# Kernel tuning notes

Measured on AMD Instinct MI355X. Metric: run time of the kernel, lower is better.

## Reference

```python
import jax, jax.numpy as jnp
import numpy as np

N, E, D = 100000, 1600000, 128
EPS = 1e-5


def _bn(h, g, b):
    m = h.mean(0)
    v = ((h - m) ** 2).mean(0)  # biased var, as torch BatchNorm1d normalization
    return g * (h - m) / jnp.sqrt(v + EPS) + b


def _sage(x, src, dst, w_self, w_neigh, b, n):
    # mean aggregation over in-neighbors (edges src->dst)
    agg = jax.ops.segment_sum(x[src], dst, num_segments=n)          # [N, D]
    cnt = jax.ops.segment_sum(jnp.ones(src.shape, x.dtype), dst, num_segments=n)
    mean = agg / jnp.maximum(cnt, 1.0)[:, None]
    return x @ w_self + mean @ w_neigh + b


def setup_inputs() -> dict:
    key = jax.random.key(0)
    ks = jax.random.split(key, 8)
    s = 1.0 / np.sqrt(D)
    return {
        "x": jax.random.normal(ks[0], (N, D), jnp.float32),
        "src": jax.random.randint(ks[1], (E,), 0, N, jnp.int32),
        "dst": jax.random.randint(ks[2], (E,), 0, N, jnp.int32),
        "w_self1": jax.random.normal(ks[3], (D, D), jnp.float32) * s,
        "w_neigh1": jax.random.normal(ks[4], (D, D), jnp.float32) * s,
        "b1": jnp.zeros((D,), jnp.float32),
        "w_self2": jax.random.normal(ks[5], (D, D), jnp.float32) * s,
        "w_neigh2": jax.random.normal(ks[6], (D, D), jnp.float32) * s,
        "b2": jnp.zeros((D,), jnp.float32),
        "w_skip": jax.random.normal(ks[7], (D, D), jnp.float32) * s,
        "b_skip": jnp.zeros((D,), jnp.float32),
        "g1": jnp.ones((D,), jnp.float32), "be1": jnp.zeros((D,), jnp.float32),
        "g2": jnp.ones((D,), jnp.float32), "be2": jnp.zeros((D,), jnp.float32),
        "g3": jnp.ones((D,), jnp.float32), "be3": jnp.zeros((D,), jnp.float32),
    }


def reference(x, src, dst, w_self1, w_neigh1, b1, w_self2, w_neigh2, b2,
              w_skip, b_skip, g1, be1, g2, be2, g3, be3):
    n = x.shape[0]
    h1 = _sage(x, src, dst, w_self1, w_neigh1, b1, n)
    h1 = jax.nn.relu(_bn(h1, g1, be1))           # dropout: eval-mode identity
    h2 = _sage(h1, src, dst, w_self2, w_neigh2, b2, n)
    h2 = _bn(h2, g2, be2)
    skip = _bn(h1 @ w_skip + b_skip, g3, be3)
    return jax.nn.relu(h2 + skip)
```

## Files before the change

kernel.cpp:

```cpp
#include <hip/hip_runtime.h>

#define D 128
#define PCHUNK 4096
#define SCAP 8192

typedef short bf16x8 __attribute__((ext_vector_type(8)));
typedef float f32x4 __attribute__((ext_vector_type(4)));

__device__ __forceinline__ ushort f2b(float f){
  unsigned u = __builtin_bit_cast(unsigned, f);
  u += 0x7fffu + ((u >> 16) & 1u);
  return (ushort)(u >> 16);
}
__device__ __forceinline__ float b2f(ushort h){
  unsigned u = ((unsigned)h) << 16;
  return __builtin_bit_cast(float, u);
}

__global__ __launch_bounds__(256) void k_p0(const int* __restrict__ dst,
                                            int* __restrict__ bcnt, int E){
  __shared__ int h[512];
  for (int u=threadIdx.x; u<512; u+=256) h[u]=0;
  __syncthreads();
  for (long long i=(long long)blockIdx.x*256+threadIdx.x; i<E; i+=(long long)gridDim.x*256)
    atomicAdd(&h[dst[i]>>8], 1);
  __syncthreads();
  for (int u=threadIdx.x; u<512; u+=256) if (h[u]) atomicAdd(&bcnt[u], h[u]);
}

__global__ void k_bscan(const int* __restrict__ bcnt, int* __restrict__ bbase,
                        int* __restrict__ bcur, int nb, int E){
  __shared__ int sh[1024];
  int t = threadIdx.x;
  int v = (t<nb) ? bcnt[t] : 0;
  sh[t]=v; __syncthreads();
  for (int off=1; off<1024; off<<=1){
    int add = (t>=off)?sh[t-off]:0;
    __syncthreads();
    sh[t]+=add;
    __syncthreads();
  }
  if (t<nb){ int e=sh[t]-v; bbase[t]=e; bcur[t]=e; }
  if (t==nb) bbase[t]=E;
}

__global__ __launch_bounds__(256) void k_part(const int* __restrict__ src,
        const int* __restrict__ dst, int* __restrict__ bcur,
        unsigned* __restrict__ pairs, int E){
  __shared__ int hist[512], offA[512], offB[512], gbase[512];
  __shared__ int sS[PCHUNK], sD[PCHUNK];
  const int t = threadIdx.x;
  const int base = blockIdx.x * PCHUNK;
  const int cnt = min(PCHUNK, E - base);
  for (int u=t; u<512; u+=256) hist[u]=0;
  __syncthreads();
  int rs[16], rd[16];
  #pragma unroll
  for (int j=0;j<16;j++){
    int li = j*256 + t;
    if (li < cnt){
      rs[j]=src[base+li]; rd[j]=dst[base+li];
      atomicAdd(&hist[rd[j]>>8],1);
    } else { rs[j]=0; rd[j]=-1; }
  }
  __syncthreads();
  int *cur=offA, *nxt=offB;
  for (int u=t; u<512; u+=256) cur[u]=hist[u];
  __syncthreads();
  for (int off=1; off<512; off<<=1){
    for (int u=t; u<512; u+=256) nxt[u] = cur[u] + ((u>=off)?cur[u-off]:0);
    __syncthreads();
    int* tmp=cur; cur=nxt; nxt=tmp;
  }
  for (int u=t; u<512; u+=256) nxt[u] = cur[u]-hist[u];
  __syncthreads();
  #pragma unroll
  for (int j=0;j<16;j++){
    if (j*256+t < cnt){
      int b = rd[j]>>8;
      int p = atomicAdd(&nxt[b],1);
      sS[p]=rs[j]; sD[p]=rd[j];
    }
  }
  __syncthreads();
  for (int u=t; u<512; u+=256){
    int c = hist[u];
    if (c>0) gbase[u] = atomicAdd(&bcur[u], c);
  }
  __syncthreads();
  #pragma unroll
  for (int j=0;j<16;j++){
    int idx = j*256+t;
    if (idx<cnt){
      int d = sD[idx]; int b = d>>8;
      int gpos = gbase[b] + (idx - (cur[b]-hist[b]));
      pairs[gpos] = (unsigned)sS[idx] | ((unsigned)(d & 255) << 24);
    }
  }
}

__global__ __launch_bounds__(256) void k_sortb(const unsigned* __restrict__ pairs,
        const int* __restrict__ bbase, int* __restrict__ offs,
        int* __restrict__ slots, int N, int NB){
  __shared__ int nh[256], nc[256], sc[256];
  __shared__ int stage[SCAP];
  const int b = blockIdx.x, t = threadIdx.x;
  const int base = bbase[b];
  const int cnt  = bbase[b+1] - base;
  nh[t]=0; __syncthreads();
  for (int i=t;i<cnt;i+=256) atomicAdd(&nh[pairs[base+i] >> 24],1);
  __syncthreads();
  int v = nh[t];
  sc[t]=v; __syncthreads();
  for (int off=1; off<256; off<<=1){
    int add = (t>=off)?sc[t-off]:0;
    __syncthreads();
    sc[t]+=add;
    __syncthreads();
  }
  int excl = sc[t]-v;
  nc[t]=excl;
  int node = (b<<8)+t;
  if (node<N) offs[node]=base+excl;
  if (b==NB-1 && t==0) offs[N]=bbase[NB];
  __syncthreads();
  if (cnt<=SCAP){
    for (int i=t;i<cnt;i+=256){
      unsigned p = pairs[base+i];
      int pos = atomicAdd(&nc[p >> 24],1);
      stage[pos]=(int)(p & 0xffffffu);
    }
    __syncthreads();
    for (int i=t;i<cnt;i+=256) slots[base+i]=stage[i];
  } else {
    for (int i=t;i<cnt;i+=256){
      unsigned p = pairs[base+i];
      int pos = atomicAdd(&nc[p >> 24],1);
      slots[base+pos]=(int)(p & 0xffffffu);
    }
  }
}

__global__ __launch_bounds__(256) void k_xcast(const float* __restrict__ x,
                                               ushort* __restrict__ xb, long long n4){
  long long i = (long long)blockIdx.x*256 + threadIdx.x;
  const long long stride = (long long)gridDim.x*256;
  for (; i < n4; i += stride){
    float4 v = reinterpret_cast<const float4*>(x)[i];
    ushort4 o;
    o.x = f2b(v.x); o.y = f2b(v.y); o.z = f2b(v.z); o.w = f2b(v.w);
    reinterpret_cast<ushort4*>(xb)[i] = o;
  }
}

__global__ __launch_bounds__(256) void k_wtall(
    const float* __restrict__ w_self1, const float* __restrict__ w_neigh1,
    const float* __restrict__ w_self2, const float* __restrict__ w_neigh2,
    const float* __restrict__ w_skip,
    ushort* __restrict__ Wb1, ushort* __restrict__ Wb2, ushort* __restrict__ Wb3){
  const int grp = blockIdx.x >> 6;
  const int idx = (blockIdx.x & 63)*256 + threadIdx.x;
  const int k = idx >> 7, c = idx & 127;
  const float* W; ushort* Wb; int K, k0;
  switch (grp){
    case 0: W=w_self1;  Wb=Wb1; K=256; k0=0;   break;
    case 1: W=w_neigh1; Wb=Wb1; K=256; k0=128; break;
    case 2: W=w_self2;  Wb=Wb2; K=256; k0=0;   break;
    case 3: W=w_neigh2; Wb=Wb2; K=256; k0=128; break;
    default:W=w_skip;   Wb=Wb3; K=128; k0=0;   break;
  }
  Wb[(size_t)c*K + k0 + k] = f2b(W[idx]);
}

__global__ __launch_bounds__(256) void k_gatherb(const ushort* __restrict__ Xb,
        const int* __restrict__ slots, const int* __restrict__ offs,
        ushort* __restrict__ meanb, int N){
  int node = blockIdx.x*4 + (threadIdx.x >> 6);
  int c2 = (threadIdx.x & 63) * 2;
  if (node >= N) return;
  const int beg = offs[node], end = offs[node+1];
  float sx0=0,sy0=0,sx1=0,sy1=0,sx2=0,sy2=0,sx3=0,sy3=0;
  int j = beg;
  while (j < end && (j & 3)){
    unsigned u = *reinterpret_cast<const unsigned*>(&Xb[(size_t)slots[j]*D + c2]);
    sx0 += b2f((ushort)u); sy0 += b2f((ushort)(u>>16));
    ++j;
  }
  const int nfull = (end - j) >> 2;
  const int4* sp = reinterpret_cast<const int4*>(slots + j);

#define G8(ia, ib) { \
    unsigned u0 = *reinterpret_cast<const unsigned*>(&Xb[(size_t)(ia).x*D + c2]); \
    unsigned u1 = *reinterpret_cast<const unsigned*>(&Xb[(size_t)(ia).y*D + c2]); \
    unsigned u2 = *reinterpret_cast<const unsigned*>(&Xb[(size_t)(ia).z*D + c2]); \
    unsigned u3 = *reinterpret_cast<const unsigned*>(&Xb[(size_t)(ia).w*D + c2]); \
    unsigned u4 = *reinterpret_cast<const unsigned*>(&Xb[(size_t)(ib).x*D + c2]); \
    unsigned u5 = *reinterpret_cast<const unsigned*>(&Xb[(size_t)(ib).y*D + c2]); \
    unsigned u6 = *reinterpret_cast<const unsigned*>(&Xb[(size_t)(ib).z*D + c2]); \
    unsigned u7 = *reinterpret_cast<const unsigned*>(&Xb[(size_t)(ib).w*D + c2]); \
    sx0 += b2f((ushort)u0); sy0 += b2f((ushort)(u0>>16)); \
    sx1 += b2f((ushort)u1); sy1 += b2f((ushort)(u1>>16)); \
    sx2 += b2f((ushort)u2); sy2 += b2f((ushort)(u2>>16)); \
    sx3 += b2f((ushort)u3); sy3 += b2f((ushort)(u3>>16)); \
    sx0 += b2f((ushort)u4); sy0 += b2f((ushort)(u4>>16)); \
    sx1 += b2f((ushort)u5); sy1 += b2f((ushort)(u5>>16)); \
    sx2 += b2f((ushort)u6); sy2 += b2f((ushort)(u6>>16)); \
    sx3 += b2f((ushort)u7); sy3 += b2f((ushort)(u7>>16)); }

  int g = 0;
  if (nfull >= 2){
    int4 ia = sp[0], ib = sp[1];
    for (g = 2; g + 2 <= nfull; g += 2){
      int4 na = sp[g], nb = sp[g+1];
      G8(ia, ib);
      ia = na; ib = nb;
    }
    G8(ia, ib);
  }
  if (g < nfull){
    int4 ia = sp[g];
    unsigned u0 = *reinterpret_cast<const unsigned*>(&Xb[(size_t)ia.x*D + c2]);
    unsigned u1 = *reinterpret_cast<const unsigned*>(&Xb[(size_t)ia.y*D + c2]);
    unsigned u2 = *reinterpret_cast<const unsigned*>(&Xb[(size_t)ia.z*D + c2]);
    unsigned u3 = *reinterpret_cast<const unsigned*>(&Xb[(size_t)ia.w*D + c2]);
    sx0 += b2f((ushort)u0); sy0 += b2f((ushort)(u0>>16));
    sx1 += b2f((ushort)u1); sy1 += b2f((ushort)(u1>>16));
    sx2 += b2f((ushort)u2); sy2 += b2f((ushort)(u2>>16));
    sx3 += b2f((ushort)u3); sy3 += b2f((ushort)(u3>>16));
  }
  j += 4*nfull;
  for (; j < end; ++j){
    unsigned u = *reinterpret_cast<const unsigned*>(&Xb[(size_t)slots[j]*D + c2]);
    sx0 += b2f((ushort)u); sy0 += b2f((ushort)(u>>16));
  }
#undef G8
  float deg = (float)(end - beg);
  float rc = deg > 0.f ? 1.0f/deg : 0.f;
  unsigned o = (unsigned)f2b((sx0+sx1+sx2+sx3)*rc)
             | ((unsigned)f2b((sy0+sy1+sy2+sy3)*rc) << 16);
  *reinterpret_cast<unsigned*>(&meanb[(size_t)node*D + c2]) = o;
}

template<bool SKIP>
__global__ __launch_bounds__(256, 2) void k_mfma(
    const ushort* __restrict__ A0, const ushort* __restrict__ A1,
    const ushort* __restrict__ Wb, const ushort* __restrict__ Wk,
    const float* __restrict__ bias, const float* __restrict__ biasK,
    ushort* __restrict__ C, ushort* __restrict__ Ck,
    float* __restrict__ gS, float* __restrict__ gQ,
    float* __restrict__ gSK, float* __restrict__ gQK, int N, int NT)
{
  __shared__ ushort At[2][64][40];
  __shared__ ushort Wt[2][128][40];
  __shared__ ushort Wkt[SKIP ? 2*128*40 : 1];
  __shared__ float shS[128], shQ[128], shSK[SKIP?128:1], shQK[SKIP?128:1];
  const int tid = threadIdx.x;
  if (tid < 128){ shS[tid]=0.f; shQ[tid]=0.f; if (SKIP){ shSK[tid]=0.f; shQK[tid]=0.f; } }
  const int bid = blockIdx.x, gridN = gridDim.x;
  const int lane = tid & 63, wid = tid >> 6;
  const int wr = wid >> 1, wc = wid & 1;
  const int lr = lane & 15, kq = lane >> 4;
  const int srA = tid >> 2, s8A = (tid & 3) * 8;
  const int srW = tid >> 2, s8W = (tid & 3) * 8;

  int4 va0, va1, va2, va3;
  int4 w0a,w0b, w1a,w1b, w2a,w2b, w3a,w3b;
  int4 k0a,k0b, k1a,k1b, k2a,k2b, k3a,k3b;

#define LOADSET(S, GT, TT) { \
    int grow_ = (GT)*64 + srA; if (grow_ >= N) grow_ = N-1; \
    const ushort* As_ = ((TT) >= 4) ? A1 : A0; \
    va##S = *reinterpret_cast<const int4*>(&As_[(size_t)grow_*D + ((TT)&3)*32 + s8A]); \
    w##S##a = *reinterpret_cast<const int4*>(&Wb[(size_t)srW*256 + (TT)*32 + s8W]); \
    w##S##b = *reinterpret_cast<const int4*>(&Wb[(size_t)(srW+64)*256 + (TT)*32 + s8W]); \
    if (SKIP && (TT) < 4){ \
      k##S##a = *reinterpret_cast<const int4*>(&Wk[(size_t)srW*128 + (TT)*32 + s8W]); \
      k##S##b = *reinterpret_cast<const int4*>(&Wk[(size_t)(srW+64)*128 + (TT)*32 + s8W]); \
    } }

#define WRITESET(S, BW, TT) { \
    *reinterpret_cast<int4*>(&At[BW][srA][s8A]) = va##S; \
    *reinterpret_cast<int4*>(&Wt[BW][srW][s8W]) = w##S##a; \
    *reinterpret_cast<int4*>(&Wt[BW][srW+64][s8W]) = w##S##b; \
    if (SKIP && (TT) < 4){ \
      *reinterpret_cast<int4*>(&Wkt[((BW)*128 + srW)*40 + s8W]) = k##S##a; \
      *reinterpret_cast<int4*>(&Wkt[((BW)*128 + srW + 64)*40 + s8W]) = k##S##b; \
    } }

#define PBAR() { asm volatile("s_waitcnt lgkmcnt(0)" ::: "memory"); \
    __builtin_amdgcn_s_barrier(); __builtin_amdgcn_sched_barrier(0); }

#define STEPBODY(BR, WITHK, ...) { \
    bf16x8 af0 = *reinterpret_cast<const bf16x8*>(&At[BR][32*wr + lr][kq*8]); \
    bf16x8 af1 = *reinterpret_cast<const bf16x8*>(&At[BR][32*wr + 16 + lr][kq*8]); \
    bf16x8 bw0 = *reinterpret_cast<const bf16x8*>(&Wt[BR][64*wc + lr][kq*8]); \
    bf16x8 bw1 = *reinterpret_cast<const bf16x8*>(&Wt[BR][64*wc + 16 + lr][kq*8]); \
    bf16x8 bw2 = *reinterpret_cast<const bf16x8*>(&Wt[BR][64*wc + 32 + lr][kq*8]); \
    bf16x8 bw3 = *reinterpret_cast<const bf16x8*>(&Wt[BR][64*wc + 48 + lr][kq*8]); \
    bf16x8 bk0{}, bk1{}, bk2{}, bk3{}; \
    if (SKIP && (WITHK)){ \
      bk0 = *reinterpret_cast<const bf16x8*>(&Wkt[((BR)*128 + 64*wc + lr)*40 + kq*8]); \
      bk1 = *reinterpret_cast<const bf16x8*>(&Wkt[((BR)*128 + 64*wc + 16 + lr)*40 + kq*8]); \
      bk2 = *reinterpret_cast<const bf16x8*>(&Wkt[((BR)*128 + 64*wc + 32 + lr)*40 + kq*8]); \
      bk3 = *reinterpret_cast<const bf16x8*>(&Wkt[((BR)*128 + 64*wc + 48 + lr)*40 + kq*8]); \
    } \
    __VA_ARGS__; \
    __builtin_amdgcn_s_setprio(1); \
    acc[0][0] = __builtin_amdgcn_mfma_f32_16x16x32_bf16(af0, bw0, acc[0][0], 0,0,0); \
    acc[0][1] = __builtin_amdgcn_mfma_f32_16x16x32_bf16(af0, bw1, acc[0][1], 0,0,0); \
    acc[0][2] = __builtin_amdgcn_mfma_f32_16x16x32_bf16(af0, bw2, acc[0][2], 0,0,0); \
    acc[0][3] = __builtin_amdgcn_mfma_f32_16x16x32_bf16(af0, bw3, acc[0][3], 0,0,0); \
    acc[1][0] = __builtin_amdgcn_mfma_f32_16x16x32_bf16(af1, bw0, acc[1][0], 0,0,0); \
    acc[1][1] = __builtin_amdgcn_mfma_f32_16x16x32_bf16(af1, bw1, acc[1][1], 0,0,0); \
    acc[1][2] = __builtin_amdgcn_mfma_f32_16x16x32_bf16(af1, bw2, acc[1][2], 0,0,0); \
    acc[1][3] = __builtin_amdgcn_mfma_f32_16x16x32_bf16(af1, bw3, acc[1][3], 0,0,0); \
    if (SKIP && (WITHK)){ \
      accK[0][0] = __builtin_amdgcn_mfma_f32_16x16x32_bf16(af0, bk0, accK[0][0], 0,0,0); \
      accK[0][1] = __builtin_amdgcn_mfma_f32_16x16x32_bf16(af0, bk1, accK[0][1], 0,0,0); \
      accK[0][2] = __builtin_amdgcn_mfma_f32_16x16x32_bf16(af0, bk2, accK[0][2], 0,0,0); \
      accK[0][3] = __builtin_amdgcn_mfma_f32_16x16x32_bf16(af0, bk3, accK[0][3], 0,0,0); \
      accK[1][0] = __builtin_amdgcn_mfma_f32_16x16x32_bf16(af1, bk0, accK[1][0], 0,0,0); \
      accK[1][1] = __builtin_amdgcn_mfma_f32_16x16x32_bf16(af1, bk1, accK[1][1], 0,0,0); \
      accK[1][2] = __builtin_amdgcn_mfma_f32_16x16x32_bf16(af1, bk2, accK[1][2], 0,0,0); \
      accK[1][3] = __builtin_amdgcn_mfma_f32_16x16x32_bf16(af1, bk3, accK[1][3], 0,0,0); \
    } \
    __builtin_amdgcn_s_setprio(0); }

  f32x4 acc[2][4], accK[SKIP?2:1][SKIP?4:1];
  #pragma unroll
  for (int m=0;m<2;m++)
    #pragma unroll
    for (int n=0;n<4;n++){
      acc[m][n] = (f32x4){0.f,0.f,0.f,0.f};
      if (SKIP) accK[m][n] = (f32x4){0.f,0.f,0.f,0.f};
    }
  float bs[4]={0,0,0,0}, bq[4]={0,0,0,0}, bsk[4]={0,0,0,0}, bqk[4]={0,0,0,0};
  float bv[4], bkv[4];
  #pragma unroll
  for (int n=0;n<4;n++){
    bv[n] = bias[64*wc + 16*n + lr];
    bkv[n] = SKIP ? biasK[64*wc + 16*n + lr] : 0.f;
  }

  {
    const int t0 = bid;
    LOADSET(0, t0, 0);
    LOADSET(1, t0, 1);
    LOADSET(2, t0, 2);
    LOADSET(3, t0, 3);
    WRITESET(0, 0, 0);
    PBAR();
  }

  for (int tile = bid; tile < NT; tile += gridN){
    const int tnext = tile + gridN;
    const bool hasnext = (tnext < NT);
    STEPBODY(0, 1, LOADSET(0, tile, 4));
    WRITESET(1, 1, 1); PBAR();
    STEPBODY(1, 1, LOADSET(1, tile, 5));
    WRITESET(2, 0, 2); PBAR();
    STEPBODY(0, 1, LOADSET(2, tile, 6));
    WRITESET(3, 1, 3); PBAR();
    STEPBODY(1, 1, LOADSET(3, tile, 7));
    WRITESET(0, 0, 4); PBAR();
    STEPBODY(0, 0, if (hasnext) LOADSET(0, tnext, 0));
    WRITESET(1, 1, 5); PBAR();
    STEPBODY(1, 0, if (hasnext) LOADSET(1, tnext, 1));
    WRITESET(2, 0, 6); PBAR();
    STEPBODY(0, 0, if (hasnext) LOADSET(2, tnext, 2));
    WRITESET(3, 1, 7); PBAR();
    STEPBODY(1, 0, if (hasnext) LOADSET(3, tnext, 3));
    if (hasnext){ WRITESET(0, 0, 0); PBAR(); }

    #pragma unroll
    for (int m=0;m<2;m++){
      #pragma unroll
      for (int r=0;r<4;r++){
        int row = tile*64 + 32*wr + 16*m + kq*4 + r;
        if (row < N){
          #pragma unroll
          for (int n=0;n<4;n++){
            int col = 64*wc + 16*n + lr;
            float v = acc[m][n][r] + bv[n];
            C[(size_t)row*D + col] = f2b(v);
            bs[n] += v; bq[n] += v*v;
            if (SKIP){
              float u = accK[m][n][r] + bkv[n];
              Ck[(size_t)row*D + col] = f2b(u);
              bsk[n] += u; bqk[n] += u*u;
            }
          }
        }
      }
    }
    #pragma unroll
    for (int m=0;m<2;m++)
      #pragma unroll
      for (int n=0;n<4;n++){
        acc[m][n] = (f32x4){0.f,0.f,0.f,0.f};
        if (SKIP) accK[m][n] = (f32x4){0.f,0.f,0.f,0.f};
      }
  }
#undef LOADSET
#undef WRITESET
#undef PBAR
#undef STEPBODY

  #pragma unroll
  for (int n=0;n<4;n++){
    float s = bs[n], q = bq[n];
    s += __shfl_xor(s,16); s += __shfl_xor(s,32);
    q += __shfl_xor(q,16); q += __shfl_xor(q,32);
    if (kq == 0){
      int col = 64*wc + 16*n + lr;
      atomicAdd(&shS[col], s);
      atomicAdd(&shQ[col], q);
    }
    if (SKIP){
      float sk = bsk[n], qk = bqk[n];
      sk += __shfl_xor(sk,16); sk += __shfl_xor(sk,32);
      qk += __shfl_xor(qk,16); qk += __shfl_xor(qk,32);
      if (kq == 0){
        int col = 64*wc + 16*n + lr;
        atomicAdd(&shSK[col], sk);
        atomicAdd(&shQK[col], qk);
      }
    }
  }
  __syncthreads();
  if (tid < 128){
    unsafeAtomicAdd(&gS[tid], shS[tid]);
    unsafeAtomicAdd(&gQ[tid], shQ[tid]);
    if (SKIP){
      unsafeAtomicAdd(&gSK[tid], shSK[tid]);
      unsafeAtomicAdd(&gQK[tid], shQK[tid]);
    }
  }
}

__global__ __launch_bounds__(256) void k_bnrelub(const ushort* __restrict__ hpre,
      ushort* __restrict__ hb,
      const float* __restrict__ sum, const float* __restrict__ sq,
      const float* __restrict__ g, const float* __restrict__ be,
      float invN, long long n4){
  __shared__ float A[128], B[128];
  if (threadIdx.x < 128){
    int c = threadIdx.x;
    float m = sum[c]*invN;
    float v = sq[c]*invN - m*m;
    float a = g[c]*rsqrtf(fmaxf(v, 0.f) + 1e-5f);
    A[c] = a;
    B[c] = be[c] - m*a;
  }
  __syncthreads();
  long long i = (long long)blockIdx.x*256 + threadIdx.x;
  const long long stride = (long long)gridDim.x*256;
  for (; i < n4; i += stride){
    int c = ((int)(i & 31)) << 2;
    float4 a = *reinterpret_cast<const float4*>(A + c);
    float4 b = *reinterpret_cast<const float4*>(B + c);
    ushort4 hv = reinterpret_cast<const ushort4*>(hpre)[i];
    ushort4 o;
    o.x = f2b(fmaxf(a.x*b2f(hv.x) + b.x, 0.f));
    o.y = f2b(fmaxf(a.y*b2f(hv.y) + b.y, 0.f));
    o.z = f2b(fmaxf(a.z*b2f(hv.z) + b.z, 0.f));
    o.w = f2b(fmaxf(a.w*b2f(hv.w) + b.w, 0.f));
    reinterpret_cast<ushort4*>(hb)[i] = o;
  }
}

__global__ __launch_bounds__(256) void k_final(const ushort* __restrict__ h2,
      const ushort* __restrict__ sk, float* __restrict__ out,
      const float* __restrict__ sum2, const float* __restrict__ sq2,
      const float* __restrict__ g2, const float* __restrict__ be2,
      const float* __restrict__ sum3, const float* __restrict__ sq3,
      const float* __restrict__ g3, const float* __restrict__ be3,
      float invN, long long n4){
  __shared__ float A2[128], B2[128], A3[128], B3[128];
  if (threadIdx.x < 128){
    int c = threadIdx.x;
    float m2 = sum2[c]*invN;
    float v2 = sq2[c]*invN - m2*m2;
    float a2 = g2[c]*rsqrtf(fmaxf(v2, 0.f) + 1e-5f);
    A2[c] = a2; B2[c] = be2[c] - m2*a2;
    float m3 = sum3[c]*invN;
    float v3 = sq3[c]*invN - m3*m3;
    float a3 = g3[c]*rsqrtf(fmaxf(v3, 0.f) + 1e-5f);
    A3[c] = a3; B3[c] = be3[c] - m3*a3;
  }
  __syncthreads();
  long long i = (long long)blockIdx.x*256 + threadIdx.x;
  const long long stride = (long long)gridDim.x*256;
  for (; i < n4; i += stride){
    int c = ((int)(i & 31)) << 2;
    float4 a2 = *reinterpret_cast<const float4*>(A2 + c);
    float4 b2 = *reinterpret_cast<const float4*>(B2 + c);
    float4 a3 = *reinterpret_cast<const float4*>(A3 + c);
    float4 b3 = *reinterpret_cast<const float4*>(B3 + c);
    ushort4 h = reinterpret_cast<const ushort4*>(h2)[i];
    ushort4 s = reinterpret_cast<const ushort4*>(sk)[i];
    float4 v;
    v.x = fmaxf(a2.x*b2f(h.x) + b2.x + a3.x*b2f(s.x) + b3.x, 0.f);
    v.y = fmaxf(a2.y*b2f(h.y) + b2.y + a3.y*b2f(s.y) + b3.y, 0.f);
    v.z = fmaxf(a2.z*b2f(h.z) + b2.z + a3.z*b2f(s.z) + b3.z, 0.f);
    v.w = fmaxf(a2.w*b2f(h.w) + b2.w + a3.w*b2f(s.w) + b3.w, 0.f);
    reinterpret_cast<float4*>(out)[i] = v;
  }
}

extern "C" void kernel_launch(void* const* d_in, const int* in_sizes, int n_in,
                              void* d_out, int out_size, void* d_ws, size_t ws_size,
                              hipStream_t stream) {
  const float* x        = (const float*)d_in[0];
  const int*   src      = (const int*)  d_in[1];
  const int*   dst      = (const int*)  d_in[2];
  const float* w_self1  = (const float*)d_in[3];
  const float* w_neigh1 = (const float*)d_in[4];
  const float* b1       = (const float*)d_in[5];
  const float* w_self2  = (const float*)d_in[6];
  const float* w_neigh2 = (const float*)d_in[7];
  const float* b2       = (const float*)d_in[8];
  const float* w_skip   = (const float*)d_in[9];
  const float* b_skip   = (const float*)d_in[10];
  const float* g1       = (const float*)d_in[11];
  const float* be1      = (const float*)d_in[12];
  const float* g2       = (const float*)d_in[13];
  const float* be2      = (const float*)d_in[14];
  const float* g3       = (const float*)d_in[15];
  const float* be3      = (const float*)d_in[16];
  (void)n_in; (void)ws_size;

  const int N = in_sizes[0] / D;
  const int E = in_sizes[1];
  const int NB = (N + 255) >> 8;
  float* out = (float*)d_out;

  char* p = (char*)d_ws;
  const size_t nd2 = (((size_t)N * D * 2) + 255) / 256 * 256;
  ushort* meanb  = (ushort*)p; p += nd2;
  ushort* h1b    = (ushort*)p; p += nd2;
  ushort* hpre_b = (ushort*)p; p += nd2;
  ushort* skip_b = (ushort*)p; p += nd2;
  ushort* Wb1    = (ushort*)p; p += 256*128*2;
  ushort* Wb2    = (ushort*)p; p += 256*128*2;
  ushort* Wb3    = (ushort*)p; p += 128*128*2;
  int*    offs   = (int*)p;   p += (((size_t)(N+1)*4) + 255) / 256 * 256;
  int*    bcnt   = (int*)p;   p += 2304;
  float*  st     = (float*)p; p += 1536*sizeof(float);
  int*    bbase  = (int*)p;   p += 2304;
  int*    bcur   = (int*)p;   p += 2048;
  float *sum1=st,      *sq1=st+128,  *sum2=st+256, *sq2=st+384, *sum3=st+512, *sq3=st+640;

  const size_t slpad = (((size_t)E*4) + 255) / 256 * 256;
  const size_t xbpad = (((size_t)N*D*2) + 255) / 256 * 256;
  int*      slots = (int*)d_out;
  ushort*   xb    = (ushort*)((char*)d_out + slpad);
  unsigned* pairs = (unsigned*)((char*)d_out + slpad + xbpad);

  hipMemsetAsync(bcnt, 0, 2304 + 1536*sizeof(float), stream);

  const long long n4 = (long long)N * D / 4;

  k_xcast<<<2048, 256, 0, stream>>>(x, xb, n4);
  k_wtall<<<320, 256, 0, stream>>>(w_self1, w_neigh1, w_self2, w_neigh2, w_skip,
                                   Wb1, Wb2, Wb3);

  k_p0<<<1024, 256, 0, stream>>>(dst, bcnt, E);
  k_bscan<<<1, 1024, 0, stream>>>(bcnt, bbase, bcur, NB, E);
  k_part<<<(E + PCHUNK - 1)/PCHUNK, 256, 0, stream>>>(src, dst, bcur, pairs, E);
  k_sortb<<<NB, 256, 0, stream>>>(pairs, bbase, offs, slots, N, NB);

  const int gablocks = (N + 3) / 4;
  const int NT = (N + 63) / 64;
  const int gpersist = 512;
  const float invN = 1.0f / (float)N;

  k_gatherb<<<gablocks, 256, 0, stream>>>(xb, slots, offs, meanb, N);
  k_mfma<false><<<gpersist, 256, 0, stream>>>(xb, meanb, Wb1, nullptr, b1, nullptr,
                                              hpre_b, nullptr, sum1, sq1, nullptr, nullptr, N, NT);
  k_bnrelub<<<4096, 256, 0, stream>>>(hpre_b, h1b, sum1, sq1, g1, be1, invN, n4);

  k_gatherb<<<gablocks, 256, 0, stream>>>(h1b, slots, offs, meanb, N);

  k_mfma<true><<<gpersist, 256, 0, stream>>>(h1b, meanb, Wb2, Wb3, b2, b_skip,
                                             hpre_b, skip_b, sum2, sq2, sum3, sq3, N, NT);

  k_final<<<4096, 256, 0, stream>>>(hpre_b, skip_b, out,
                                    sum2, sq2, g2, be2, sum3, sq3, g3, be3, invN, n4);
}
```

Measured before the change: 301.3 us.

## Keep weights resident in LDS and double MFMA row tile to 128

The persistent GEMM kernel now loads the full concatenated weight matrix (and the skip weight) into LDS once per block, instead of streaming weight slices alongside every A tile. The row tile grows from 64 to 128 rows, so each wave computes a 64x64 output block with twice the accumulators. The grid is halved to 256 blocks and launch bounds drop to one block per CU. This cuts redundant global weight loads and LDS writes per tile, at the cost of a large LDS footprint (about 100 KB with skip) and higher register pressure, which lowers occupancy.

```diff
diff --git a/kernel.cpp b/kernel.cpp
--- a/kernel.cpp
+++ b/kernel.cpp
@@ -242,7 +242,7 @@
 }
 
 template<bool SKIP>
-__global__ __launch_bounds__(256, 2) void k_mfma(
+__global__ __launch_bounds__(256, 1) void k_mfma(
     const ushort* __restrict__ A0, const ushort* __restrict__ A1,
     const ushort* __restrict__ Wb, const ushort* __restrict__ Wk,
     const float* __restrict__ bias, const float* __restrict__ biasK,
@@ -250,9 +250,9 @@
     float* __restrict__ gS, float* __restrict__ gQ,
     float* __restrict__ gSK, float* __restrict__ gQK, int N, int NT)
 {
-  __shared__ ushort At[2][64][40];
-  __shared__ ushort Wt[2][128][40];
-  __shared__ ushort Wkt[SKIP ? 2*128*40 : 1];
+  __shared__ ushort Wt8[8][128][40];
+  __shared__ ushort Wkt4[SKIP ? 4*128*40 : 1];
+  __shared__ ushort At[2][128][40];
   __shared__ float shS[128], shQ[128], shSK[SKIP?128:1], shQK[SKIP?128:1];
   const int tid = threadIdx.x;
   if (tid < 128){ shS[tid]=0.f; shQ[tid]=0.f; if (SKIP){ shSK[tid]=0.f; shQK[tid]=0.f; } }
@@ -260,49 +260,57 @@
   const int lane = tid & 63, wid = tid >> 6;
   const int wr = wid >> 1, wc = wid & 1;
   const int lr = lane & 15, kq = lane >> 4;
-  const int srA = tid >> 2, s8A = (tid & 3) * 8;
-  const int srW = tid >> 2, s8W = (tid & 3) * 8;
-
-  int4 va0, va1, va2, va3;
-  int4 w0a,w0b, w1a,w1b, w2a,w2b, w3a,w3b;
-  int4 k0a,k0b, k1a,k1b, k2a,k2b, k3a,k3b;
-
-#define LOADSET(S, GT, TT) { \
-    int grow_ = (GT)*64 + srA; if (grow_ >= N) grow_ = N-1; \
+  const int sr4 = tid >> 2, s8 = (tid & 3) * 8;
+
+  #pragma unroll
+  for (int s=0;s<8;s++){
+    *reinterpret_cast<int4*>(&Wt8[s][sr4][s8]) =
+        *reinterpret_cast<const int4*>(&Wb[(size_t)sr4*256 + s*32 + s8]);
+    *reinterpret_cast<int4*>(&Wt8[s][sr4+64][s8]) =
+        *reinterpret_cast<const int4*>(&Wb[(size_t)(sr4+64)*256 + s*32 + s8]);
+  }
+  if (SKIP){
+    #pragma unroll
+    for (int s=0;s<4;s++){
+      *reinterpret_cast<int4*>(&Wkt4[((s*128) + sr4)*40 + s8]) =
+          *reinterpret_cast<const int4*>(&Wk[(size_t)sr4*128 + s*32 + s8]);
+      *reinterpret_cast<int4*>(&Wkt4[((s*128) + sr4 + 64)*40 + s8]) =
+          *reinterpret_cast<const int4*>(&Wk[(size_t)(sr4+64)*128 + s*32 + s8]);
+    }
+  }
+
+  int4 va0a,va0b, va1a,va1b, va2a,va2b, va3a,va3b;
+
+#define LOADA(S, GT, TT) { \
+    int gr0_ = (GT)*128 + sr4;      if (gr0_ >= N) gr0_ = N-1; \
+    int gr1_ = (GT)*128 + sr4 + 64; if (gr1_ >= N) gr1_ = N-1; \
     const ushort* As_ = ((TT) >= 4) ? A1 : A0; \
-    va##S = *reinterpret_cast<const int4*>(&As_[(size_t)grow_*D + ((TT)&3)*32 + s8A]); \
-    w##S##a = *reinterpret_cast<const int4*>(&Wb[(size_t)srW*256 + (TT)*32 + s8W]); \
-    w##S##b = *reinterpret_cast<const int4*>(&Wb[(size_t)(srW+64)*256 + (TT)*32 + s8W]); \
-    if (SKIP && (TT) < 4){ \
-      k##S##a = *reinterpret_cast<const int4*>(&Wk[(size_t)srW*128 + (TT)*32 + s8W]); \
-      k##S##b = *reinterpret_cast<const int4*>(&Wk[(size_t)(srW+64)*128 + (TT)*32 + s8W]); \
-    } }
-
-#define WRITESET(S, BW, TT) { \
-    *reinterpret_cast<int4*>(&At[BW][srA][s8A]) = va##S; \
-    *reinterpret_cast<int4*>(&Wt[BW][srW][s8W]) = w##S##a; \
-    *reinterpret_cast<int4*>(&Wt[BW][srW+64][s8W]) = w##S##b; \
-    if (SKIP && (TT) < 4){ \
-      *reinterpret_cast<int4*>(&Wkt[((BW)*128 + srW)*40 + s8W]) = k##S##a; \
-      *reinterpret_cast<int4*>(&Wkt[((BW)*128 + srW + 64)*40 + s8W]) = k##S##b; \
-    } }
+    const int ka_ = ((TT) & 3) * 32; \
+    va##S##a = *reinterpret_cast<const int4*>(&As_[(size_t)gr0_*D + ka_ + s8]); \
+    va##S##b = *reinterpret_cast<const int4*>(&As_[(size_t)gr1_*D + ka_ + s8]); }
+
+#define WRITEA(S, BW) { \
+    *reinterpret_cast<int4*>(&At[BW][sr4][s8]) = va##S##a; \
+    *reinterpret_cast<int4*>(&At[BW][sr4+64][s8]) = va##S##b; }
 
 #define PBAR() { asm volatile("s_waitcnt lgkmcnt(0)" ::: "memory"); \
     __builtin_amdgcn_s_barrier(); __builtin_amdgcn_sched_barrier(0); }
 
-#define STEPBODY(BR, WITHK, ...) { \
-    bf16x8 af0 = *reinterpret_cast<const bf16x8*>(&At[BR][32*wr + lr][kq*8]); \
-    bf16x8 af1 = *reinterpret_cast<const bf16x8*>(&At[BR][32*wr + 16 + lr][kq*8]); \
-    bf16x8 bw0 = *reinterpret_cast<const bf16x8*>(&Wt[BR][64*wc + lr][kq*8]); \
-    bf16x8 bw1 = *reinterpret_cast<const bf16x8*>(&Wt[BR][64*wc + 16 + lr][kq*8]); \
-    bf16x8 bw2 = *reinterpret_cast<const bf16x8*>(&Wt[BR][64*wc + 32 + lr][kq*8]); \
-    bf16x8 bw3 = *reinterpret_cast<const bf16x8*>(&Wt[BR][64*wc + 48 + lr][kq*8]); \
+#define STEPBODY(BR, TT, WITHK, ...) { \
+    bf16x8 af0 = *reinterpret_cast<const bf16x8*>(&At[BR][64*wr + lr][kq*8]); \
+    bf16x8 af1 = *reinterpret_cast<const bf16x8*>(&At[BR][64*wr + 16 + lr][kq*8]); \
+    bf16x8 af2 = *reinterpret_cast<const bf16x8*>(&At[BR][64*wr + 32 + lr][kq*8]); \
+    bf16x8 af3 = *reinterpret_cast<const bf16x8*>(&At[BR][64*wr + 48 + lr][kq*8]); \
+    bf16x8 bw0 = *reinterpret_cast<const bf16x8*>(&Wt8[TT][64*wc + lr][kq*8]); \
+    bf16x8 bw1 = *reinterpret_cast<const bf16x8*>(&Wt8[TT][64*wc + 16 + lr][kq*8]); \
+    bf16x8 bw2 = *reinterpret_cast<const bf16x8*>(&Wt8[TT][64*wc + 32 + lr][kq*8]); \
+    bf16x8 bw3 = *reinterpret_cast<const bf16x8*>(&Wt8[TT][64*wc + 48 + lr][kq*8]); \
     bf16x8 bk0{}, bk1{}, bk2{}, bk3{}; \
     if (SKIP && (WITHK)){ \
-      bk0 = *reinterpret_cast<const bf16x8*>(&Wkt[((BR)*128 + 64*wc + lr)*40 + kq*8]); \
-      bk1 = *reinterpret_cast<const bf16x8*>(&Wkt[((BR)*128 + 64*wc + 16 + lr)*40 + kq*8]); \
-      bk2 = *reinterpret_cast<const bf16x8*>(&Wkt[((BR)*128 + 64*wc + 32 + lr)*40 + kq*8]); \
-      bk3 = *reinterpret_cast<const bf16x8*>(&Wkt[((BR)*128 + 64*wc + 48 + lr)*40 + kq*8]); \
+      bk0 = *reinterpret_cast<const bf16x8*>(&Wkt4[(((TT)&3)*128 + 64*wc + lr)*40 + kq*8]); \
+      bk1 = *reinterpret_cast<const bf16x8*>(&Wkt4[(((TT)&3)*128 + 64*wc + 16 + lr)*40 + kq*8]); \
+      bk2 = *reinterpret_cast<const bf16x8*>(&Wkt4[(((TT)&3)*128 + 64*wc + 32 + lr)*40 + kq*8]); \
+      bk3 = *reinterpret_cast<const bf16x8*>(&Wkt4[(((TT)&3)*128 + 64*wc + 48 + lr)*40 + kq*8]); \
     } \
     __VA_ARGS__; \
     __builtin_amdgcn_s_setprio(1); \
@@ -314,6 +322,14 @@
     acc[1][1] = __builtin_amdgcn_mfma_f32_16x16x32_bf16(af1, bw1, acc[1][1], 0,0,0); \
     acc[1][2] = __builtin_amdgcn_mfma_f32_16x16x32_bf16(af1, bw2, acc[1][2], 0,0,0); \
     acc[1][3] = __builtin_amdgcn_mfma_f32_16x16x32_bf16(af1, bw3, acc[1][3], 0,0,0); \
+    acc[2][0] = __builtin_amdgcn_mfma_f32_16x16x32_bf16(af2, bw0, acc[2][0], 0,0,0); \
+    acc[2][1] = __builtin_amdgcn_mfma_f32_16x16x32_bf16(af2, bw1, acc[2][1], 0,0,0); \
+    acc[2][2] = __builtin_amdgcn_mfma_f32_16x16x32_bf16(af2, bw2, acc[2][2], 0,0,0); \
+    acc[2][3] = __builtin_amdgcn_mfma_f32_16x16x32_bf16(af2, bw3, acc[2][3], 0,0,0); \
+    acc[3][0] = __builtin_amdgcn_mfma_f32_16x16x32_bf16(af3, bw0, acc[3][0], 0,0,0); \
+    acc[3][1] = __builtin_amdgcn_mfma_f32_16x16x32_bf16(af3, bw1, acc[3][1], 0,0,0); \
+    acc[3][2] = __builtin_amdgcn_mfma_f32_16x16x32_bf16(af3, bw2, acc[3][2], 0,0,0); \
+    acc[3][3] = __builtin_amdgcn_mfma_f32_16x16x32_bf16(af3, bw3, acc[3][3], 0,0,0); \
     if (SKIP && (WITHK)){ \
       accK[0][0] = __builtin_amdgcn_mfma_f32_16x16x32_bf16(af0, bk0, accK[0][0], 0,0,0); \
       accK[0][1] = __builtin_amdgcn_mfma_f32_16x16x32_bf16(af0, bk1, accK[0][1], 0,0,0); \
@@ -323,12 +339,20 @@
       accK[1][1] = __builtin_amdgcn_mfma_f32_16x16x32_bf16(af1, bk1, accK[1][1], 0,0,0); \
       accK[1][2] = __builtin_amdgcn_mfma_f32_16x16x32_bf16(af1, bk2, accK[1][2], 0,0,0); \
       accK[1][3] = __builtin_amdgcn_mfma_f32_16x16x32_bf16(af1, bk3, accK[1][3], 0,0,0); \
+      accK[2][0] = __builtin_amdgcn_mfma_f32_16x16x32_bf16(af2, bk0, accK[2][0], 0,0,0); \
+      accK[2][1] = __builtin_amdgcn_mfma_f32_16x16x32_bf16(af2, bk1, accK[2][1], 0,0,0); \
+      accK[2][2] = __builtin_amdgcn_mfma_f32_16x16x32_bf16(af2, bk2, accK[2][2], 0,0,0); \
+      accK[2][3] = __builtin_amdgcn_mfma_f32_16x16x32_bf16(af2, bk3, accK[2][3], 0,0,0); \
+      accK[3][0] = __builtin_amdgcn_mfma_f32_16x16x32_bf16(af3, bk0, accK[3][0], 0,0,0); \
+      accK[3][1] = __builtin_amdgcn_mfma_f32_16x16x32_bf16(af3, bk1, accK[3][1], 0,0,0); \
+      accK[3][2] = __builtin_amdgcn_mfma_f32_16x16x32_bf16(af3, bk2, accK[3][2], 0,0,0); \
+      accK[3][3] = __builtin_amdgcn_mfma_f32_16x16x32_bf16(af3, bk3, accK[3][3], 0,0,0); \
     } \
     __builtin_amdgcn_s_setprio(0); }
 
-  f32x4 acc[2][4], accK[SKIP?2:1][SKIP?4:1];
+  f32x4 acc[4][4], accK[SKIP?4:1][SKIP?4:1];
   #pragma unroll
-  for (int m=0;m<2;m++)
+  for (int m=0;m<4;m++)
     #pragma unroll
     for (int n=0;n<4;n++){
       acc[m][n] = (f32x4){0.f,0.f,0.f,0.f};
@@ -344,39 +368,39 @@
 
   {
     const int t0 = bid;
-    LOADSET(0, t0, 0);
-    LOADSET(1, t0, 1);
-    LOADSET(2, t0, 2);
-    LOADSET(3, t0, 3);
-    WRITESET(0, 0, 0);
+    LOADA(0, t0, 0);
+    LOADA(1, t0, 1);
+    LOADA(2, t0, 2);
+    LOADA(3, t0, 3);
+    WRITEA(0, 0);
     PBAR();
   }
 
   for (int tile = bid; tile < NT; tile += gridN){
     const int tnext = tile + gridN;
     const bool hasnext = (tnext < NT);
-    STEPBODY(0, 1, LOADSET(0, tile, 4));
-    WRITESET(1, 1, 1); PBAR();
-    STEPBODY(1, 1, LOADSET(1, tile, 5));
-    WRITESET(2, 0, 2); PBAR();
-    STEPBODY(0, 1, LOADSET(2, tile, 6));
-    WRITESET(3, 1, 3); PBAR();
-    STEPBODY(1, 1, LOADSET(3, tile, 7));
-    WRITESET(0, 0, 4); PBAR();
-    STEPBODY(0, 0, if (hasnext) LOADSET(0, tnext, 0));
-    WRITESET(1, 1, 5); PBAR();
-    STEPBODY(1, 0, if (hasnext) LOADSET(1, tnext, 1));
-    WRITESET(2, 0, 6); PBAR();
-    STEPBODY(0, 0, if (hasnext) LOADSET(2, tnext, 2));
-    WRITESET(3, 1, 7); PBAR();
-    STEPBODY(1, 0, if (hasnext) LOADSET(3, tnext, 3));
-    if (hasnext){ WRITESET(0, 0, 0); PBAR(); }
+    STEPBODY(0, 0, 1, LOADA(0, tile, 4));
+    WRITEA(1, 1); PBAR();
+    STEPBODY(1, 1, 1, LOADA(1, tile, 5));
+    WRITEA(2, 0); PBAR();
+    STEPBODY(0, 2, 1, LOADA(2, tile, 6));
+    WRITEA(3, 1); PBAR();
+    STEPBODY(1, 3, 1, LOADA(3, tile, 7));
+    WRITEA(0, 0); PBAR();
+    STEPBODY(0, 4, 0, if (hasnext) LOADA(0, tnext, 0));
+    WRITEA(1, 1); PBAR();
+    STEPBODY(1, 5, 0, if (hasnext) LOADA(1, tnext, 1));
+    WRITEA(2, 0); PBAR();
+    STEPBODY(0, 6, 0, if (hasnext) LOADA(2, tnext, 2));
+    WRITEA(3, 1); PBAR();
+    STEPBODY(1, 7, 0, if (hasnext) LOADA(3, tnext, 3));
+    if (hasnext){ WRITEA(0, 0); PBAR(); }
 
     #pragma unroll
-    for (int m=0;m<2;m++){
+    for (int m=0;m<4;m++){
       #pragma unroll
       for (int r=0;r<4;r++){
-        int row = tile*64 + 32*wr + 16*m + kq*4 + r;
+        int row = tile*128 + 64*wr + 16*m + kq*4 + r;
         if (row < N){
           #pragma unroll
           for (int n=0;n<4;n++){
@@ -394,15 +418,15 @@
       }
     }
     #pragma unroll
-    for (int m=0;m<2;m++)
+    for (int m=0;m<4;m++)
       #pragma unroll
       for (int n=0;n<4;n++){
         acc[m][n] = (f32x4){0.f,0.f,0.f,0.f};
         if (SKIP) accK[m][n] = (f32x4){0.f,0.f,0.f,0.f};
       }
   }
-#undef LOADSET
-#undef WRITESET
+#undef LOADA
+#undef WRITEA
 #undef PBAR
 #undef STEPBODY
 
@@ -571,8 +595,8 @@
   k_sortb<<<NB, 256, 0, stream>>>(pairs, bbase, offs, slots, N, NB);
 
   const int gablocks = (N + 3) / 4;
-  const int NT = (N + 63) / 64;
-  const int gpersist = 512;
+  const int NT = (N + 127) / 128;
+  const int gpersist = 256;
   const float invN = 1.0f / (float)N;
 
   k_gatherb<<<gablocks, 256, 0, stream>>>(xb, slots, offs, meanb, N);
```

Measured after the change: 292.1 us. 3.0% less time.
